# Optimization experiments

Measured on AMD Instinct MI355X. Metric: run time of the kernel, lower is better.

Reference implementation:

```python
import jax, jax.numpy as jnp
import numpy as np
import math

B, S, H = 2, 2048, 2048
NH, HD = 16, 128
THETA = 10000.0
NEG = -1e9


def make_rope_tables(seq_len, head_dim, theta):
    inv_freq = 1.0 / (theta ** (np.arange(0, head_dim, 2, dtype=np.float32) / head_dim))
    pos = np.arange(seq_len, dtype=np.float32)
    freqs = np.outer(pos, inv_freq)                    # (S, HD/2)
    emb = np.concatenate([freqs, freqs], axis=-1)      # (S, HD)
    return jnp.asarray(np.cos(emb)), jnp.asarray(np.sin(emb))


def setup_inputs() -> dict:
    key = jax.random.key(0)
    k1, k2, k3 = jax.random.split(key, 3)
    hidden_states = jax.random.normal(k1, (B, S, H), dtype=jnp.float32)
    rope_cos, rope_sin = make_rope_tables(S, HD, THETA)
    # additive causal mask [1,1,S,S]
    causal = jnp.tril(jnp.ones((S, S), dtype=bool))
    attention_mask = jnp.where(causal, 0.0, NEG).astype(jnp.float32)[None, None]
    w_qkv = jax.random.normal(k2, (3 * H, H), dtype=jnp.float32) * (1.0 / math.sqrt(H))
    w_o = jax.random.normal(k3, (H, H), dtype=jnp.float32) * (1.0 / math.sqrt(H))
    return {"hidden_states": hidden_states, "rope_cos": rope_cos, "rope_sin": rope_sin,
            "attention_mask": attention_mask, "w_qkv": w_qkv, "w_o": w_o}


def apply_rope(x, cos, sin):
    # x: (B, NH, S, HD); cos/sin: (S, HD)
    half = x.shape[-1] // 2
    x1, x2 = x[..., :half], x[..., half:]
    x_rot = jnp.concatenate([-x2, x1], axis=-1)
    return x * cos[None, None] + x_rot * sin[None, None]


def reference(hidden_states, rope_cos, rope_sin, attention_mask, w_qkv, w_o):
    b, s, h = hidden_states.shape
    qkv = hidden_states @ w_qkv.T                      # (B, S, 3H)
    qkv = qkv.reshape(b, s, 3, NH, HD).transpose(2, 0, 3, 1, 4)  # (3, B, NH, S, HD)
    q, k, v = qkv[0], qkv[1], qkv[2]
    q = apply_rope(q, rope_cos, rope_sin)
    k = apply_rope(k, rope_cos, rope_sin)
    scale = 1.0 / math.sqrt(HD)
    scores = jnp.einsum('bhqd,bhkd->bhqk', q, k) * scale + attention_mask
    probs = jax.nn.softmax(scores.astype(jnp.float32), axis=-1).astype(q.dtype)
    out = jnp.einsum('bhqk,bhkd->bhqd', probs, v)      # (B, NH, S, HD)
    out = out.transpose(0, 2, 1, 3).reshape(b, s, h)
    return out @ w_o.T
```

## Files before the change

### kernel.cpp

```cpp
#include <hip/hip_runtime.h>
#include <stdint.h>

typedef unsigned int u32;
typedef unsigned short u16;

typedef __bf16 bf16x8 __attribute__((ext_vector_type(8)));
typedef float f32x4 __attribute__((ext_vector_type(4)));

struct alignas(16) V16 { u32 a, b, c, d; };

__device__ __forceinline__ u16 f2bf(float x) {
    u32 u = __float_as_uint(x);
    u += 0x7FFFu + ((u >> 16) & 1u);
    return (u16)(u >> 16);
}
__device__ __forceinline__ float bf2f(u16 h) {
    return __uint_as_float(((u32)h) << 16);
}

__device__ __forceinline__ bf16x8 ld_frag(const u16* p) {
    return __builtin_bit_cast(bf16x8, *(const V16*)p);
}

__device__ __forceinline__ void async_cp16(u16* lds_dst, const u16* g_src) {
    __builtin_amdgcn_global_load_lds(
        (__attribute__((address_space(1))) void*)g_src,
        (__attribute__((address_space(3))) void*)lds_dst, 16, 0, 0);
}

__global__ __launch_bounds__(256) void cast_bf16_kernel(
    const float* __restrict__ in, u16* __restrict__ out, int n4)
{
    int i = blockIdx.x * 256 + threadIdx.x;
    if (i >= n4) return;
    const float* p = in + (size_t)i * 4;
    ushort4 o;
    o.x = f2bf(p[0]); o.y = f2bf(p[1]); o.z = f2bf(p[2]); o.w = f2bf(p[3]);
    *(ushort4*)(out + (size_t)i * 4) = o;
}

__global__ __launch_bounds__(256) void gemm_bt(
    const u16* __restrict__ A, const u16* __restrict__ Bt,
    int M, int N, int K, int mode,
    float* __restrict__ Cout,
    u16* __restrict__ Qb, u16* __restrict__ Kb, u16* __restrict__ Vtb)
{
    __shared__ u16 As[128 * 32];
    __shared__ u16 Bs[128 * 32];

    const int t = threadIdx.x;
    const int w = t >> 6, l = t & 63;
    const int lr = l & 15;
    const int lk = (l >> 4) * 8;
    const int m0 = blockIdx.y * 128, n0 = blockIdx.x * 128;
    const int wm = (w >> 1) * 64, wn = (w & 1) * 64;

    f32x4 acc[4][4];
#pragma unroll
    for (int i = 0; i < 4; ++i)
#pragma unroll
        for (int j = 0; j < 4; ++j) acc[i][j] = f32x4{0.f, 0.f, 0.f, 0.f};

    const u16* Ag = A + (size_t)m0 * K;
    const u16* Bg = Bt + (size_t)n0 * K;
    const int srow = t >> 2;
    const int scol = (t & 3) * 8;

    for (int k0 = 0; k0 < K; k0 += 32) {
        async_cp16(&As[(size_t)(w * 64) * 8],         Ag + (size_t)srow * K + k0 + scol);
        async_cp16(&As[(size_t)(256 + w * 64) * 8],   Ag + (size_t)(64 + srow) * K + k0 + scol);
        async_cp16(&Bs[(size_t)(w * 64) * 8],         Bg + (size_t)srow * K + k0 + scol);
        async_cp16(&Bs[(size_t)(256 + w * 64) * 8],   Bg + (size_t)(64 + srow) * K + k0 + scol);
        __syncthreads();

        bf16x8 af[4], bf[4];
#pragma unroll
        for (int i = 0; i < 4; ++i) af[i] = ld_frag(&As[(wm + i * 16 + lr) * 32 + lk]);
#pragma unroll
        for (int j = 0; j < 4; ++j) bf[j] = ld_frag(&Bs[(wn + j * 16 + lr) * 32 + lk]);
#pragma unroll
        for (int i = 0; i < 4; ++i)
#pragma unroll
            for (int j = 0; j < 4; ++j)
                acc[i][j] = __builtin_amdgcn_mfma_f32_16x16x32_bf16(af[i], bf[j], acc[i][j], 0, 0, 0);
        __syncthreads();
    }

    const int lrow4 = (l >> 4) * 4;
    if (mode == 1) {
#pragma unroll
        for (int i = 0; i < 4; ++i)
#pragma unroll
            for (int j = 0; j < 4; ++j)
#pragma unroll
                for (int r = 0; r < 4; ++r) {
                    int gr = m0 + wm + i * 16 + lrow4 + r;
                    int gc = n0 + wn + j * 16 + lr;
                    Cout[(size_t)gr * N + gc] = acc[i][j][r];
                }
    } else {
#pragma unroll
        for (int i = 0; i < 4; ++i)
#pragma unroll
            for (int j = 0; j < 4; ++j)
#pragma unroll
                for (int r = 0; r < 4; ++r) {
                    int gr = m0 + wm + i * 16 + lrow4 + r;
                    int gc = n0 + wn + j * 16 + lr;
                    u16 hv = f2bf(acc[i][j][r]);
                    int which = gc >> 11;
                    int rem = gc & 2047;
                    int nh = rem >> 7, d = rem & 127;
                    int b = gr >> 11, s = gr & 2047;
                    size_t bhn = (size_t)b * 16 + nh;
                    if (which == 0)      Qb[(bhn * 2048 + s) * 128 + d] = hv;
                    else if (which == 1) Kb[(bhn * 2048 + s) * 128 + d] = hv;
                    else                 Vtb[(bhn * 128 + d) * 2048 + s] = hv;
                }
    }
}

__global__ __launch_bounds__(256) void rope_kernel(
    u16* __restrict__ Qb, u16* __restrict__ Kb,
    const float* __restrict__ cosT, const float* __restrict__ sinT, float qscale)
{
    int idx = blockIdx.x * 256 + threadIdx.x;
    int d = idx & 63;
    int s = (idx >> 6) & 2047;
    int bh = idx >> 17;
    size_t base = ((size_t)bh * 2048 + s) * 128;
    float c = cosT[s * 128 + d], sn = sinT[s * 128 + d];
    float q1 = bf2f(Qb[base + d]), q2 = bf2f(Qb[base + d + 64]);
    Qb[base + d]      = f2bf((q1 * c - q2 * sn) * qscale);
    Qb[base + d + 64] = f2bf((q2 * c + q1 * sn) * qscale);
    float k1 = bf2f(Kb[base + d]), k2 = bf2f(Kb[base + d + 64]);
    Kb[base + d]      = f2bf(k1 * c - k2 * sn);
    Kb[base + d + 64] = f2bf(k2 * c + k1 * sn);
}

#define PS_LD 72
__global__ __launch_bounds__(256, 2) void flash_attn(
    const u16* __restrict__ Qb, const u16* __restrict__ Kb, const u16* __restrict__ Vtb,
    u16* __restrict__ ctx)
{
    __shared__ u16 Ks[4 * 64 * 32];
    __shared__ u16 Vts[2 * 128 * 32];
    __shared__ u16 Ps[4 * 16 * PS_LD];

    const int t = threadIdx.x, w = t >> 6, l = t & 63;
    const int lr = l & 15, lk = (l >> 4) * 8, lrow4 = (l >> 4) * 4;
    const int bh = blockIdx.x;
    const int pidx = blockIdx.y;
    const int wm = w * 16;

    const u16* Qg = Qb + (size_t)bh * 2048 * 128;
    const u16* Kg = Kb + (size_t)bh * 2048 * 128;
    const u16* Vg = Vtb + (size_t)bh * 128 * 2048;
    u16* Pw = &Ps[w * 16 * PS_LD];

    const int srow = l >> 2;
    const int scol = (l & 3) * 8;
    const int vh = w & 1, vkc = w >> 1;

    const int b = bh >> 4, nh = bh & 15;

#pragma unroll
    for (int half = 0; half < 2; ++half) {
        const int qt = half ? pidx : 31 - pidx;
        const int q0 = qt * 64;

        bf16x8 qfrag[4];
#pragma unroll
        for (int kc = 0; kc < 4; ++kc)
            qfrag[kc] = ld_frag(&Qg[(size_t)(q0 + wm + lr) * 128 + kc * 32 + lk]);

        f32x4 oacc[8];
#pragma unroll
        for (int jo = 0; jo < 8; ++jo) oacc[jo] = f32x4{0.f, 0.f, 0.f, 0.f};
        float l_part[4] = {0.f, 0.f, 0.f, 0.f};

        const int ktiles = qt + 1;
        for (int kt = 0; kt < ktiles; ++kt) {
            const int c0 = kt * 64;
#pragma unroll
            for (int it = 0; it < 4; ++it)
                async_cp16(&Ks[w * 2048 + it * 512],
                           Kg + (size_t)(c0 + it * 16 + srow) * 128 + w * 32 + scol);
#pragma unroll
            for (int it = 0; it < 4; ++it)
                async_cp16(&Vts[vkc * 4096 + (vh * 64 + it * 16) * 32],
                           Vg + (size_t)(vh * 64 + it * 16 + srow) * 2048 + c0 + vkc * 32 + scol);
            __syncthreads();

            f32x4 pacc[4];
#pragma unroll
            for (int j = 0; j < 4; ++j) pacc[j] = f32x4{0.f, 0.f, 0.f, 0.f};
#pragma unroll
            for (int kc = 0; kc < 4; ++kc) {
                bf16x8 bk[4];
#pragma unroll
                for (int j = 0; j < 4; ++j)
                    bk[j] = ld_frag(&Ks[kc * 2048 + (j * 16 + lr) * 32 + lk]);
#pragma unroll
                for (int j = 0; j < 4; ++j)
                    pacc[j] = __builtin_amdgcn_mfma_f32_16x16x32_bf16(qfrag[kc], bk[j], pacc[j], 0, 0, 0);
            }

            if (kt == qt) {
#pragma unroll
                for (int j = 0; j < 4; ++j) {
                    const int cl = j * 16 + lr;
#pragma unroll
                    for (int r = 0; r < 4; ++r) {
                        float pv = (cl > wm + lrow4 + r) ? 0.f : __expf(pacc[j][r]);
                        pacc[j][r] = pv;
                        l_part[r] += pv;
                    }
                }
            } else {
#pragma unroll
                for (int j = 0; j < 4; ++j)
#pragma unroll
                    for (int r = 0; r < 4; ++r) {
                        float pv = __expf(pacc[j][r]);
                        pacc[j][r] = pv;
                        l_part[r] += pv;
                    }
            }

#pragma unroll
            for (int j = 0; j < 4; ++j)
#pragma unroll
                for (int r = 0; r < 4; ++r)
                    Pw[(lrow4 + r) * PS_LD + j * 16 + lr] = f2bf(pacc[j][r]);

#pragma unroll
            for (int kc = 0; kc < 2; ++kc) {
                bf16x8 ap = ld_frag(&Pw[lr * PS_LD + kc * 32 + lk]);
#pragma unroll
                for (int jo = 0; jo < 8; ++jo) {
                    bf16x8 bv = ld_frag(&Vts[kc * 4096 + (jo * 16 + lr) * 32 + lk]);
                    oacc[jo] = __builtin_amdgcn_mfma_f32_16x16x32_bf16(ap, bv, oacc[jo], 0, 0, 0);
                }
            }
            __syncthreads();
        }

        float linv[4];
#pragma unroll
        for (int r = 0; r < 4; ++r) {
            float s = l_part[r];
#pragma unroll
            for (int dd = 8; dd >= 1; dd >>= 1) s += __shfl_xor(s, dd);
            linv[r] = __builtin_amdgcn_rcpf(s);
        }
#pragma unroll
        for (int jo = 0; jo < 8; ++jo)
#pragma unroll
            for (int r = 0; r < 4; ++r) {
                int srow2 = q0 + wm + lrow4 + r;
                int col = nh * 128 + jo * 16 + lr;
                ctx[((size_t)b * 2048 + srow2) * 2048 + col] = f2bf(oacc[jo][r] * linv[r]);
            }
    }
}

extern "C" void kernel_launch(void* const* d_in, const int* in_sizes, int n_in,
                              void* d_out, int out_size, void* d_ws, size_t ws_size,
                              hipStream_t stream)
{
    (void)in_sizes; (void)n_in; (void)out_size; (void)ws_size;
    const float* hidden = (const float*)d_in[0];
    const float* cosT   = (const float*)d_in[1];
    const float* sinT   = (const float*)d_in[2];
    const float* wqkv   = (const float*)d_in[4];
    const float* wo     = (const float*)d_in[5];
    float* out = (float*)d_out;
    char* ws = (char*)d_ws;

    u16* hA   = (u16*)(ws + 0);
    u16* wqb  = (u16*)(ws + 16777216);
    u16* wob  = (u16*)(ws + 41943040);
    u16* Qb   = (u16*)(ws + 50331648);
    u16* Kb   = (u16*)(ws + 67108864);
    u16* Vtb  = (u16*)(ws + 83886080);
    u16* ctx  = (u16*)(ws + 100663296);

    cast_bf16_kernel<<<dim3(8192),  dim3(256), 0, stream>>>(hidden, hA, 2097152);
    cast_bf16_kernel<<<dim3(12288), dim3(256), 0, stream>>>(wqkv, wqb, 3145728);
    cast_bf16_kernel<<<dim3(4096),  dim3(256), 0, stream>>>(wo, wob, 1048576);

    gemm_bt<<<dim3(48, 32), dim3(256), 0, stream>>>(hA, wqb, 4096, 6144, 2048, 0,
                                                    nullptr, Qb, Kb, Vtb);
    rope_kernel<<<dim3(16384), dim3(256), 0, stream>>>(Qb, Kb, cosT, sinT,
                                                       0.08838834764831845f);

    flash_attn<<<dim3(32, 16), dim3(256), 0, stream>>>(Qb, Kb, Vtb, ctx);

    gemm_bt<<<dim3(16, 32), dim3(256), 0, stream>>>(ctx, wob, 4096, 2048, 2048, 1,
                                                    out, nullptr, nullptr, nullptr);
}
```

Baseline: 448.2 us.

## Merge cast kernels, deepen GEMM K-step, remap blocks per XCD, vectorize RoPE

Combines the three fp32-to-bf16 cast launches into one kernel that dispatches by index range. The GEMM now loads a 64-wide K slab per barrier pair, stored as two 32-wide sub-tiles, which halves the number of synchronisations. It also remaps block indices so each XCD handles a contiguous group of output columns for better L2 reuse. RoPE is rewritten to process 8 elements per thread with 16-byte loads and stores, using 8x fewer blocks; the trade-off is higher LDS use and more register pressure in the GEMM.

```diff
diff --git a/kernel.cpp b/kernel.cpp
--- a/kernel.cpp
+++ b/kernel.cpp
@@ -28,15 +28,20 @@
         (__attribute__((address_space(3))) void*)lds_dst, 16, 0, 0);
 }
 
-__global__ __launch_bounds__(256) void cast_bf16_kernel(
-    const float* __restrict__ in, u16* __restrict__ out, int n4)
+__global__ __launch_bounds__(256) void cast_all_kernel(
+    const float* __restrict__ hidden, const float* __restrict__ wqkv,
+    const float* __restrict__ wo,
+    u16* __restrict__ hA, u16* __restrict__ wqb, u16* __restrict__ wob)
 {
     int i = blockIdx.x * 256 + threadIdx.x;
-    if (i >= n4) return;
-    const float* p = in + (size_t)i * 4;
+    const float* src; u16* dst; int off;
+    if (i < 2097152)      { src = hidden; dst = hA;  off = i; }
+    else if (i < 5242880) { src = wqkv;   dst = wqb; off = i - 2097152; }
+    else                  { src = wo;     dst = wob; off = i - 5242880; }
+    const float* p = src + (size_t)off * 4;
     ushort4 o;
     o.x = f2bf(p[0]); o.y = f2bf(p[1]); o.z = f2bf(p[2]); o.w = f2bf(p[3]);
-    *(ushort4*)(out + (size_t)i * 4) = o;
+    *(ushort4*)(dst + (size_t)off * 4) = o;
 }
 
 __global__ __launch_bounds__(256) void gemm_bt(
@@ -45,14 +50,20 @@
     float* __restrict__ Cout,
     u16* __restrict__ Qb, u16* __restrict__ Kb, u16* __restrict__ Vtb)
 {
-    __shared__ u16 As[128 * 32];
-    __shared__ u16 Bs[128 * 32];
+    __shared__ u16 As[2 * 128 * 32];
+    __shared__ u16 Bs[2 * 128 * 32];
 
     const int t = threadIdx.x;
     const int w = t >> 6, l = t & 63;
     const int lr = l & 15;
     const int lk = (l >> 4) * 8;
-    const int m0 = blockIdx.y * 128, n0 = blockIdx.x * 128;
+
+    const int flat = blockIdx.y * gridDim.x + blockIdx.x;
+    const int xcd = flat & 7, slot = flat >> 3;
+    const int cpx = gridDim.x >> 3;
+    const int ncol = xcd * cpx + slot % cpx;
+    const int mrow = slot / cpx;
+    const int m0 = mrow * 128, n0 = ncol * 128;
     const int wm = (w >> 1) * 64, wn = (w & 1) * 64;
 
     f32x4 acc[4][4];
@@ -63,26 +74,38 @@
 
     const u16* Ag = A + (size_t)m0 * K;
     const u16* Bg = Bt + (size_t)n0 * K;
-    const int srow = t >> 2;
-    const int scol = (t & 3) * 8;
-
-    for (int k0 = 0; k0 < K; k0 += 32) {
-        async_cp16(&As[(size_t)(w * 64) * 8],         Ag + (size_t)srow * K + k0 + scol);
-        async_cp16(&As[(size_t)(256 + w * 64) * 8],   Ag + (size_t)(64 + srow) * K + k0 + scol);
-        async_cp16(&Bs[(size_t)(w * 64) * 8],         Bg + (size_t)srow * K + k0 + scol);
-        async_cp16(&Bs[(size_t)(256 + w * 64) * 8],   Bg + (size_t)(64 + srow) * K + k0 + scol);
+    const int srow = l >> 2;
+    const int scol = (l & 3) * 8;
+
+    for (int k0 = 0; k0 < K; k0 += 64) {
+#pragma unroll
+        for (int g = 0; g < 2; ++g) {
+            const int row = w * 32 + g * 16;
+#pragma unroll
+            for (int c = 0; c < 2; ++c) {
+                async_cp16(&As[c * 4096 + row * 32],
+                           Ag + (size_t)(row + srow) * K + k0 + c * 32 + scol);
+                async_cp16(&Bs[c * 4096 + row * 32],
+                           Bg + (size_t)(row + srow) * K + k0 + c * 32 + scol);
+            }
+        }
         __syncthreads();
 
-        bf16x8 af[4], bf[4];
-#pragma unroll
-        for (int i = 0; i < 4; ++i) af[i] = ld_frag(&As[(wm + i * 16 + lr) * 32 + lk]);
-#pragma unroll
-        for (int j = 0; j < 4; ++j) bf[j] = ld_frag(&Bs[(wn + j * 16 + lr) * 32 + lk]);
-#pragma unroll
-        for (int i = 0; i < 4; ++i)
+#pragma unroll
+        for (int c = 0; c < 2; ++c) {
+            bf16x8 af[4], bf[4];
+#pragma unroll
+            for (int i = 0; i < 4; ++i)
+                af[i] = ld_frag(&As[c * 4096 + (wm + i * 16 + lr) * 32 + lk]);
 #pragma unroll
             for (int j = 0; j < 4; ++j)
-                acc[i][j] = __builtin_amdgcn_mfma_f32_16x16x32_bf16(af[i], bf[j], acc[i][j], 0, 0, 0);
+                bf[j] = ld_frag(&Bs[c * 4096 + (wn + j * 16 + lr) * 32 + lk]);
+#pragma unroll
+            for (int i = 0; i < 4; ++i)
+#pragma unroll
+                for (int j = 0; j < 4; ++j)
+                    acc[i][j] = __builtin_amdgcn_mfma_f32_16x16x32_bf16(af[i], bf[j], acc[i][j], 0, 0, 0);
+        }
         __syncthreads();
     }
 
@@ -125,17 +148,35 @@
     const float* __restrict__ cosT, const float* __restrict__ sinT, float qscale)
 {
     int idx = blockIdx.x * 256 + threadIdx.x;
-    int d = idx & 63;
-    int s = (idx >> 6) & 2047;
-    int bh = idx >> 17;
+    int d = (idx & 7) * 8;
+    int s = (idx >> 3) & 2047;
+    int bh = idx >> 14;
     size_t base = ((size_t)bh * 2048 + s) * 128;
-    float c = cosT[s * 128 + d], sn = sinT[s * 128 + d];
-    float q1 = bf2f(Qb[base + d]), q2 = bf2f(Qb[base + d + 64]);
-    Qb[base + d]      = f2bf((q1 * c - q2 * sn) * qscale);
-    Qb[base + d + 64] = f2bf((q2 * c + q1 * sn) * qscale);
-    float k1 = bf2f(Kb[base + d]), k2 = bf2f(Kb[base + d + 64]);
-    Kb[base + d]      = f2bf(k1 * c - k2 * sn);
-    Kb[base + d + 64] = f2bf(k2 * c + k1 * sn);
+    float c[8], sn[8];
+#pragma unroll
+    for (int i = 0; i < 8; ++i) {
+        c[i]  = cosT[s * 128 + d + i];
+        sn[i] = sinT[s * 128 + d + i];
+    }
+    union U { V16 v; u16 h[8]; };
+    U qlo, qhi, klo, khi, a, bq, ak, bk;
+    qlo.v = *(const V16*)&Qb[base + d];
+    qhi.v = *(const V16*)&Qb[base + d + 64];
+    klo.v = *(const V16*)&Kb[base + d];
+    khi.v = *(const V16*)&Kb[base + d + 64];
+#pragma unroll
+    for (int i = 0; i < 8; ++i) {
+        float q1 = bf2f(qlo.h[i]), q2 = bf2f(qhi.h[i]);
+        a.h[i]  = f2bf((q1 * c[i] - q2 * sn[i]) * qscale);
+        bq.h[i] = f2bf((q2 * c[i] + q1 * sn[i]) * qscale);
+        float k1 = bf2f(klo.h[i]), k2 = bf2f(khi.h[i]);
+        ak.h[i] = f2bf(k1 * c[i] - k2 * sn[i]);
+        bk.h[i] = f2bf(k2 * c[i] + k1 * sn[i]);
+    }
+    *(V16*)&Qb[base + d]      = a.v;
+    *(V16*)&Qb[base + d + 64] = bq.v;
+    *(V16*)&Kb[base + d]      = ak.v;
+    *(V16*)&Kb[base + d + 64] = bk.v;
 }
 
 #define PS_LD 72
@@ -286,14 +327,13 @@
     u16* Vtb  = (u16*)(ws + 83886080);
     u16* ctx  = (u16*)(ws + 100663296);
 
-    cast_bf16_kernel<<<dim3(8192),  dim3(256), 0, stream>>>(hidden, hA, 2097152);
-    cast_bf16_kernel<<<dim3(12288), dim3(256), 0, stream>>>(wqkv, wqb, 3145728);
-    cast_bf16_kernel<<<dim3(4096),  dim3(256), 0, stream>>>(wo, wob, 1048576);
+    cast_all_kernel<<<dim3(24576), dim3(256), 0, stream>>>(hidden, wqkv, wo,
+                                                           hA, wqb, wob);
 
     gemm_bt<<<dim3(48, 32), dim3(256), 0, stream>>>(hA, wqb, 4096, 6144, 2048, 0,
                                                     nullptr, Qb, Kb, Vtb);
-    rope_kernel<<<dim3(16384), dim3(256), 0, stream>>>(Qb, Kb, cosT, sinT,
-                                                       0.08838834764831845f);
+    rope_kernel<<<dim3(2048), dim3(256), 0, stream>>>(Qb, Kb, cosT, sinT,
+                                                      0.08838834764831845f);
 
     flash_attn<<<dim3(32, 16), dim3(256), 0, stream>>>(Qb, Kb, Vtb, ctx);
 
```

New measurement: 423.0 us. 1.06x faster.
